# Kernel tuning notes

Measured on AMD Instinct MI355X. Metric: run time of the kernel, lower is better.

The kernel has to match this reference:

```python
import jax, jax.numpy as jnp
import numpy as np

NLAT, NLON = 361, 720
LMAX = NLAT - 1          # lobatto grid: lmax = nlat - 1
MMAX = NLON // 2 + 1     # rfft width


def setup_inputs() -> dict:
    key = jax.random.key(0)
    kx, kw = jax.random.split(key)
    x = jax.random.normal(kx, (1, 8, NLAT, NLON), dtype=jnp.float32)
    # Precomputed quadrature-weighted associated Legendre table [mmax, lmax, nlat].
    # Faithful structure: P_l^m == 0 for l < m (triangular in (m, l)).
    w = jax.random.normal(kw, (MMAX, LMAX, NLAT), dtype=jnp.float32)
    tri = (jnp.arange(LMAX)[None, :, None] >= jnp.arange(MMAX)[:, None, None])
    weights = w * tri.astype(jnp.float32)
    return {"x": x, "weights": weights}


def reference(x, weights):
    nlon = x.shape[-1]
    mmax = weights.shape[0]
    # torch.fft.rfft(..., norm='forward') scales by 1/nlon; module multiplies by 2*pi
    X = (2.0 * jnp.pi / nlon) * jnp.fft.rfft(x, axis=-1)   # [..., nlat, nlon//2+1] complex
    X = X[..., :mmax]                                       # [..., k=nlat, m=mmax]
    # out[..., l, m] = sum_k X[..., k, m] * W[m, l, k]  (applied to real & imag parts)
    out = jnp.einsum('...km,mlk->...lm', X, weights.astype(X.real.dtype))
    return out  # complex64, shape [..., lmax, mmax]
```

## Files before the change

kernel.cpp:

```cpp
#include <hip/hip_runtime.h>

#define NLAT 361
#define NLON 720
#define LMAX 360
#define MMAX 361

#define NS   6
#define QN   61
#define NN   64
#define XTQ_FLOATS (MMAX * NLAT * 8)

static constexpr float kAngF = 8.72664625997164788e-3f;

__global__ __launch_bounds__(256) void k_dft4(const float* __restrict__ x,
                                              float* __restrict__ xtq) {
    const int bx  = blockIdx.x;
    const int nq  = blockIdx.y;
    const int tid = threadIdx.x;
    const int ks  = tid >> 7;
    const int ml  = tid & 127;
    const int n0  = nq * QN;

    __shared__ __align__(16) float xe[2][NN][8];

    for (int j = tid; j < 2 * 8 * NN; j += 256) {
        int s  = j / (8 * NN);
        int r  = j - s * (8 * NN);
        int ch = r / NN;
        int nn = r - ch * NN;
        int n  = n0 + nn;
        int k  = bx * 2 + s;
        float v = 0.f;
        if (nn < QN && n <= 360 && k <= 360) {
            const float* __restrict__ row = x + ((size_t)ch * NLAT + k) * NLON;
            float a = row[n];
            float b = (n == 0) ? 0.f : row[NLON - n];
            v = a + b;
        }
        xe[s][nn][ch] = v;
    }
    __syncthreads();

    int mm[3];
    mm[0] = ml; mm[1] = ml + 128;
    const bool m2v = (ml + 256 <= 360);
    mm[2] = m2v ? (ml + 256) : 360;

    float P0[3], P1[3], c2[3];
#pragma unroll
    for (int q = 0; q < 3; ++q) {
        int m  = mm[q];
        int t0 = (n0 * m) % NLON;
        int t1 = t0 + m; if (t1 >= NLON) t1 -= NLON;
        P0[q] = cosf((float)t0 * kAngF);
        P1[q] = cosf((float)t1 * kAngF);
        c2[q] = 2.f * cosf((float)m * kAngF);
    }

    float acc[3][8];
#pragma unroll
    for (int q = 0; q < 3; ++q)
#pragma unroll
        for (int b = 0; b < 8; ++b) acc[q][b] = 0.f;

#pragma unroll 4
    for (int nn = 0; nn < NN; ++nn) {
        float4 e0 = *(const float4*)&xe[ks][nn][0];
        float4 e1 = *(const float4*)&xe[ks][nn][4];
#pragma unroll
        for (int q = 0; q < 3; ++q) {
            float f = P0[q];
            acc[q][0] += f * e0.x;  acc[q][1] += f * e0.y;
            acc[q][2] += f * e0.z;  acc[q][3] += f * e0.w;
            acc[q][4] += f * e1.x;  acc[q][5] += f * e1.y;
            acc[q][6] += f * e1.z;  acc[q][7] += f * e1.w;
            float Pn = c2[q] * P1[q] - P0[q];
            P0[q] = P1[q];
            P1[q] = Pn;
        }
    }

    if (nq == NS - 1) {
        float4 e0 = *(const float4*)&xe[ks][55][0];
        float4 e1 = *(const float4*)&xe[ks][55][4];
#pragma unroll
        for (int q = 0; q < 3; ++q) {
            float sgn = (mm[q] & 1) ? -1.f : 1.f;
            float h = 0.5f * sgn;
            acc[q][0] -= h * e0.x;  acc[q][1] -= h * e0.y;
            acc[q][2] -= h * e0.z;  acc[q][3] -= h * e0.w;
            acc[q][4] -= h * e1.x;  acc[q][5] -= h * e1.y;
            acc[q][6] -= h * e1.z;  acc[q][7] -= h * e1.w;
        }
    }

#pragma unroll
    for (int q = 0; q < 3; ++q)
#pragma unroll
        for (int b = 0; b < 8; ++b) acc[q][b] *= kAngF;

    const int k = bx * 2 + ks;
    if (k <= 360) {
        float4* __restrict__ o4 = (float4*)(xtq + (size_t)nq * XTQ_FLOATS);
        int b0 = (mm[0] * NLAT + k) * 2;
        o4[b0]     = make_float4(acc[0][0], acc[0][1], acc[0][2], acc[0][3]);
        o4[b0 + 1] = make_float4(acc[0][4], acc[0][5], acc[0][6], acc[0][7]);
        int b1 = (mm[1] * NLAT + k) * 2;
        o4[b1]     = make_float4(acc[1][0], acc[1][1], acc[1][2], acc[1][3]);
        o4[b1 + 1] = make_float4(acc[1][4], acc[1][5], acc[1][6], acc[1][7]);
        if (m2v) {
            int b2 = (mm[2] * NLAT + k) * 2;
            o4[b2]     = make_float4(acc[2][0], acc[2][1], acc[2][2], acc[2][3]);
            o4[b2 + 1] = make_float4(acc[2][4], acc[2][5], acc[2][6], acc[2][7]);
        }
    }
}

__global__ __launch_bounds__(256) void k_reduce6(const float* __restrict__ q,
                                                 float4* __restrict__ o) {
    int i = blockIdx.x * 256 + threadIdx.x;
    if (i >= XTQ_FLOATS / 4) return;
    const float4* q4 = (const float4*)q;
    float4 s = q4[i];
#pragma unroll
    for (int u = 1; u < NS; ++u) {
        float4 a = q4[i + (size_t)u * (XTQ_FLOATS / 4)];
        s.x += a.x; s.y += a.y; s.z += a.z; s.w += a.w;
    }
    o[i] = s;
}

__global__ __launch_bounds__(256) void k_contract4(const float* __restrict__ W,
                                                   const float* __restrict__ xt,
                                                   float* __restrict__ out) {
    const int lt   = blockIdx.x;
    const int mloc = blockIdx.y;
    const int m    = mloc;
    const int l0   = lt * 32;
    const int tid  = threadIdx.x;

    if (l0 + 31 < m) {
        int l = l0 + (tid >> 3), bc = tid & 7;
        out[(bc * LMAX + l) * MMAX + m] = 0.f;
        return;
    }

    const int kk = tid & 31, lq = tid >> 5;
    const int lb = l0 + lq * 4;

    int lr[4];
#pragma unroll
    for (int j = 0; j < 4; ++j) {
        int l = lb + j;
        if (l < m)        l = m;
        if (l > LMAX - 1) l = LMAX - 1;
        lr[j] = l;
    }

    const float* __restrict__ Wm = W + (size_t)m * (LMAX * NLAT);
    const float* __restrict__ r0 = Wm + lr[0] * NLAT + kk;
    const float* __restrict__ r1 = Wm + lr[1] * NLAT + kk;
    const float* __restrict__ r2 = Wm + lr[2] * NLAT + kk;
    const float* __restrict__ r3 = Wm + lr[3] * NLAT + kk;

    float wv[12][4];
#pragma unroll
    for (int t = 0; t < 11; ++t) {
        wv[t][0] = r0[t * 32];
        wv[t][1] = r1[t * 32];
        wv[t][2] = r2[t * 32];
        wv[t][3] = r3[t * 32];
    }
    {
        int kq = 11 * 32 + kk;
        int kc = (kq <= 360) ? kq : 360;
        wv[11][0] = Wm[lr[0] * NLAT + kc];
        wv[11][1] = Wm[lr[1] * NLAT + kc];
        wv[11][2] = Wm[lr[2] * NLAT + kc];
        wv[11][3] = Wm[lr[3] * NLAT + kc];
        if (kq > 360) { wv[11][0] = wv[11][1] = wv[11][2] = wv[11][3] = 0.f; }
    }

    float v[32];
#pragma unroll
    for (int i = 0; i < 32; ++i) v[i] = 0.f;

    const float4* __restrict__ xt4 = (const float4*)xt;
#pragma unroll
    for (int t = 0; t < 12; ++t) {
        int kq = t * 32 + kk;
        int kc = (kq <= 360) ? kq : 360;
        int xb = (mloc * NLAT + kc) * 2;
        float4 x0 = xt4[xb], x1 = xt4[xb + 1];
#pragma unroll
        for (int j = 0; j < 4; ++j) {
            float wj = wv[t][j];
            v[j*8 + 0] += wj * x0.x;  v[j*8 + 1] += wj * x0.y;
            v[j*8 + 2] += wj * x0.z;  v[j*8 + 3] += wj * x0.w;
            v[j*8 + 4] += wj * x1.x;  v[j*8 + 5] += wj * x1.y;
            v[j*8 + 6] += wj * x1.z;  v[j*8 + 7] += wj * x1.w;
        }
    }

#define RSTEP(MASK, CNT) { const bool hi = (kk & MASK) != 0; \
    _Pragma("unroll") \
    for (int i = 0; i < CNT; ++i) { \
        float keep = hi ? v[i + CNT] : v[i]; \
        float send = hi ? v[i] : v[i + CNT]; \
        v[i] = keep + __shfl_xor(send, MASK); } }
    RSTEP(16, 16) RSTEP(8, 8) RSTEP(4, 4) RSTEP(2, 2) RSTEP(1, 1)
#undef RSTEP

    int j  = kk >> 3;
    int bc = kk & 7;
    int l  = l0 + lq * 4 + j;
    if (l >= LMAX) return;
    float r = (l < m) ? 0.f : v[0];
    out[(bc * LMAX + l) * MMAX + m] = r;
}

template<int CPLX>
__global__ __launch_bounds__(192) void k_dft_leg(const float* __restrict__ x,
                                                 float* __restrict__ xt,
                                                 int mb, int mc) {
    const int k    = blockIdx.x;
    const int half = blockIdx.y;
    const int tid  = threadIdx.x;

    __shared__ __align__(16) float  xr[8 * 724];
    __shared__ __align__(16) float2 exo[8 * 362];

    {
        const float4* __restrict__ x4 = (const float4*)x;
        for (int j = tid; j < 8 * 180; j += 192) {
            int b = j / 180, q = j - b * 180;
            ((float4*)&xr[b * 724])[q] = x4[(b * NLAT + k) * 180 + q];
        }
        if (tid < 8) ((float4*)&xr[tid * 724])[180] = make_float4(0.f, 0.f, 0.f, 0.f);
    }
    __syncthreads();

    for (int j = tid; j < 8 * NLAT; j += 192) {
        int b = j / NLAT, n = j - b * NLAT;
        float xa  = xr[b * 724 + n];
        float xbv = xr[b * 724 + (NLON - n)];
        exo[b * 362 + n] = make_float2(xa + xbv, xa - xbv);
    }
    __syncthreads();

    const int  m_local = half * 192 + tid;
    const bool valid   = (m_local < mc);
    const int  m       = mb + (valid ? m_local : 0);

    float aRe[8], aIm[8];
#pragma unroll
    for (int b = 0; b < 8; ++b) { aRe[b] = 0.f; aIm[b] = 0.f; }

    int tacc = 0;
    for (int n = 0; n < NLAT; ++n) {
        float sn, cs;
        __sincosf((float)tacc * kAngF, &sn, &cs);
        float wgt = (n == 360) ? 0.5f : 1.0f;
        float fc = wgt * kAngF * cs;
        float fs = -wgt * kAngF * sn;
        tacc += m;
        if (tacc >= NLON) tacc -= NLON;
#pragma unroll
        for (int b = 0; b < 8; ++b) {
            float2 e = exo[b * 362 + n];
            aRe[b] += fc * e.x;
            if (CPLX) aIm[b] += fs * e.y;
        }
    }

    if (valid) {
        float4* __restrict__ xt4 = (float4*)xt;
        if (CPLX) {
            int base = (m_local * NLAT + k) * 4;
#pragma unroll
            for (int q = 0; q < 4; ++q)
                xt4[base + q] = make_float4(aRe[2*q], aIm[2*q], aRe[2*q+1], aIm[2*q+1]);
        } else {
            int base = (m_local * NLAT + k) * 2;
            xt4[base + 0] = make_float4(aRe[0], aRe[1], aRe[2], aRe[3]);
            xt4[base + 1] = make_float4(aRe[4], aRe[5], aRe[6], aRe[7]);
        }
    }
}

template<int CPLX>
__global__ __launch_bounds__(256) void k_contract_leg(const float* __restrict__ W,
                                                      const float* __restrict__ xt,
                                                      float* __restrict__ out,
                                                      int mb) {
    const int lt   = blockIdx.x;
    const int mloc = blockIdx.y;
    const int m    = mb + mloc;
    const int l0   = lt * 32;
    const int tid  = threadIdx.x;

    if (l0 + 31 < m) {
        int l = l0 + (tid >> 3), bc = tid & 7;
        int idx = (bc * LMAX + l) * MMAX + m;
        if (CPLX) ((float2*)out)[idx] = make_float2(0.f, 0.f);
        else      out[idx] = 0.f;
        return;
    }

    const int kk = tid & 31, lq = tid >> 5;
    const int lb = l0 + lq * 4;

    int lr[4];
#pragma unroll
    for (int j = 0; j < 4; ++j) {
        int l = lb + j;
        if (l < m)        l = m;
        if (l > LMAX - 1) l = LMAX - 1;
        lr[j] = l;
    }

    const float* __restrict__ Wm = W + (size_t)m * (LMAX * NLAT);
    const float4* __restrict__ xt4 = (const float4*)xt;
    constexpr int NX = CPLX ? 4 : 2;
    constexpr int NV = CPLX ? 64 : 32;

    float v[NV];
#pragma unroll
    for (int i = 0; i < NV; ++i) v[i] = 0.f;

#define CLOAD(T, WV, XV) { \
    int kq = (T) * 32 + kk; \
    int kc = (kq < NLAT) ? kq : (NLAT - 1); \
    _Pragma("unroll") \
    for (int j = 0; j < 4; ++j) WV[j] = Wm[lr[j] * NLAT + kc]; \
    int xb = (mloc * NLAT + kc) * NX; \
    _Pragma("unroll") \
    for (int q = 0; q < NX; ++q) XV[q] = xt4[xb + q]; \
    if (kq >= NLAT) { WV[0] = WV[1] = WV[2] = WV[3] = 0.f; } }

#define CFMA(WV, XV) { \
    _Pragma("unroll") \
    for (int j = 0; j < 4; ++j) { \
        float wj = WV[j]; \
        if (CPLX) { \
            _Pragma("unroll") \
            for (int q = 0; q < 4; ++q) { \
                v[j*16 + (2*q  )*2 + 0] += wj * XV[q].x; \
                v[j*16 + (2*q  )*2 + 1] += wj * XV[q].y; \
                v[j*16 + (2*q+1)*2 + 0] += wj * XV[q].z; \
                v[j*16 + (2*q+1)*2 + 1] += wj * XV[q].w; \
            } \
        } else { \
            v[j*8 + 0] += wj * XV[0].x;  v[j*8 + 1] += wj * XV[0].y; \
            v[j*8 + 2] += wj * XV[0].z;  v[j*8 + 3] += wj * XV[0].w; \
            v[j*8 + 4] += wj * XV[1].x;  v[j*8 + 5] += wj * XV[1].y; \
            v[j*8 + 6] += wj * XV[1].z;  v[j*8 + 7] += wj * XV[1].w; \
        } \
    } }

    float  w0[4], w1[4], wn[4];
    float4 x0[NX], x1[NX], xn[NX];
    CLOAD(0, w0, x0)
    CLOAD(1, w1, x1)
#pragma unroll
    for (int t = 0; t < 12; ++t) {
        if (t < 10) CLOAD(t + 2, wn, xn)
        CFMA(w0, x0)
#pragma unroll
        for (int j = 0; j < 4; ++j) w0[j] = w1[j];
#pragma unroll
        for (int q = 0; q < NX; ++q) x0[q] = x1[q];
        if (t < 10) {
#pragma unroll
            for (int j = 0; j < 4; ++j) w1[j] = wn[j];
#pragma unroll
            for (int q = 0; q < NX; ++q) x1[q] = xn[q];
        }
    }
#undef CLOAD
#undef CFMA

#define RSTEP(MASK, CNT) { const bool hi = (kk & MASK) != 0; \
    _Pragma("unroll") \
    for (int i = 0; i < CNT; ++i) { \
        float keep = hi ? v[i + CNT] : v[i]; \
        float send = hi ? v[i] : v[i + CNT]; \
        v[i] = keep + __shfl_xor(send, MASK); } }
    if (CPLX) {
        RSTEP(16, 32) RSTEP(8, 16) RSTEP(4, 8) RSTEP(2, 4) RSTEP(1, 2)
    } else {
        RSTEP(16, 16) RSTEP(8, 8) RSTEP(4, 4) RSTEP(2, 2) RSTEP(1, 1)
    }
#undef RSTEP

    int j  = kk >> 3;
    int bc = kk & 7;
    int l  = l0 + lq * 4 + j;
    if (l >= LMAX) return;
    int idx = (bc * LMAX + l) * MMAX + m;
    if (CPLX) {
        float2 r = make_float2(v[0], v[1]);
        if (l < m) r = make_float2(0.f, 0.f);
        ((float2*)out)[idx] = r;
    } else {
        float r = (l < m) ? 0.f : v[0];
        out[idx] = r;
    }
}

extern "C" void kernel_launch(void* const* d_in, const int* in_sizes, int n_in,
                              void* d_out, int out_size, void* d_ws, size_t ws_size,
                              hipStream_t stream) {
    const float* x = (const float*)d_in[0];
    const float* W = (const float*)d_in[1];
    float* ws = (float*)d_ws;

    const int n_complex = 8 * LMAX * MMAX;
    const int cplx = (out_size >= 2 * n_complex) ? 1 : 0;

    if (!cplx) {
        const size_t need = (size_t)(NS + 1) * XTQ_FLOATS * sizeof(float);
        if (ws_size >= need) {
            float* q  = ws;
            float* xt = ws + (size_t)NS * XTQ_FLOATS;
            k_dft4<<<dim3(181, NS), dim3(256), 0, stream>>>(x, q);
            k_reduce6<<<dim3((XTQ_FLOATS / 4 + 255) / 256), dim3(256), 0, stream>>>(
                q, (float4*)xt);
            k_contract4<<<dim3(12, MMAX), dim3(256), 0, stream>>>(W, xt, (float*)d_out);
            return;
        }
    }

    const int xs_per_mk = cplx ? 16 : 8;
    const size_t per_m_bytes = (size_t)NLAT * xs_per_mk * sizeof(float);
    int CM = (int)(ws_size / per_m_bytes);
    if (CM > MMAX) CM = MMAX;
    if (CM < 1)    CM = 1;
    for (int mbase = 0; mbase < MMAX; mbase += CM) {
        int mc = MMAX - mbase;
        if (mc > CM) mc = CM;
        if (cplx) {
            k_dft_leg<1><<<dim3(NLAT, (mc + 191) / 192), dim3(192), 0, stream>>>(
                x, ws, mbase, mc);
            k_contract_leg<1><<<dim3(12, mc), dim3(256), 0, stream>>>(W, ws, (float*)d_out, mbase);
        } else {
            k_dft_leg<0><<<dim3(NLAT, (mc + 191) / 192), dim3(192), 0, stream>>>(
                x, ws, mbase, mc);
            k_contract_leg<0><<<dim3(12, mc), dim3(256), 0, stream>>>(W, ws, (float*)d_out, mbase);
        }
    }
}
```

Baseline: 54.15 us.

## Split DFT work over m instead of n and drop partial-sum reduction kernel

The real DFT kernel now assigns one m per thread across 3 m-chunks and loops over all 361 n values, instead of giving each thread three m values over one of six n-slices. This removes the six-way partial buffer and the separate reduction kernel, cutting workspace traffic and one launch. The Chebyshev recurrence restarts every ~91 steps to limit error, and it uses fast __cosf. The cost is a larger shared tile per block (361 rows instead of 64) and a longer serial loop per thread with less reuse of each shared-memory load across m values.

```diff
diff --git a/kernel.cpp b/kernel.cpp
--- a/kernel.cpp
+++ b/kernel.cpp
@@ -5,129 +5,88 @@
 #define LMAX 360
 #define MMAX 361
 
-#define NS   6
-#define QN   61
-#define NN   64
-#define XTQ_FLOATS (MMAX * NLAT * 8)
+#define XT_FLOATS (MMAX * NLAT * 8)
 
 static constexpr float kAngF = 8.72664625997164788e-3f;
 
-__global__ __launch_bounds__(256) void k_dft4(const float* __restrict__ x,
-                                              float* __restrict__ xtq) {
+__global__ __launch_bounds__(256) void k_dft5(const float* __restrict__ x,
+                                              float* __restrict__ xt) {
     const int bx  = blockIdx.x;
-    const int nq  = blockIdx.y;
+    const int mc  = blockIdx.y;
     const int tid = threadIdx.x;
     const int ks  = tid >> 7;
     const int ml  = tid & 127;
-    const int n0  = nq * QN;
-
-    __shared__ __align__(16) float xe[2][NN][8];
-
-    for (int j = tid; j < 2 * 8 * NN; j += 256) {
-        int s  = j / (8 * NN);
-        int r  = j - s * (8 * NN);
-        int ch = r / NN;
-        int nn = r - ch * NN;
-        int n  = n0 + nn;
+    const int m   = mc * 128 + ml;
+    const bool mv = (m <= 360);
+    const int mm  = mv ? m : 360;
+
+    __shared__ __align__(16) float xe[2][361][12];
+
+    for (int j = tid; j < 2 * 8 * 361; j += 256) {
+        int s  = j / 2888;
+        int r  = j - s * 2888;
+        int ch = r / 361;
+        int n  = r - ch * 361;
         int k  = bx * 2 + s;
         float v = 0.f;
-        if (nn < QN && n <= 360 && k <= 360) {
+        if (k <= 360) {
             const float* __restrict__ row = x + ((size_t)ch * NLAT + k) * NLON;
             float a = row[n];
             float b = (n == 0) ? 0.f : row[NLON - n];
             v = a + b;
         }
-        xe[s][nn][ch] = v;
+        xe[s][n][ch] = v;
     }
     __syncthreads();
 
-    int mm[3];
-    mm[0] = ml; mm[1] = ml + 128;
-    const bool m2v = (ml + 256 <= 360);
-    mm[2] = m2v ? (ml + 256) : 360;
-
-    float P0[3], P1[3], c2[3];
-#pragma unroll
-    for (int q = 0; q < 3; ++q) {
-        int m  = mm[q];
-        int t0 = (n0 * m) % NLON;
-        int t1 = t0 + m; if (t1 >= NLON) t1 -= NLON;
-        P0[q] = cosf((float)t0 * kAngF);
-        P1[q] = cosf((float)t1 * kAngF);
-        c2[q] = 2.f * cosf((float)m * kAngF);
-    }
-
-    float acc[3][8];
-#pragma unroll
-    for (int q = 0; q < 3; ++q)
-#pragma unroll
-        for (int b = 0; b < 8; ++b) acc[q][b] = 0.f;
-
-#pragma unroll 4
-    for (int nn = 0; nn < NN; ++nn) {
-        float4 e0 = *(const float4*)&xe[ks][nn][0];
-        float4 e1 = *(const float4*)&xe[ks][nn][4];
-#pragma unroll
-        for (int q = 0; q < 3; ++q) {
-            float f = P0[q];
-            acc[q][0] += f * e0.x;  acc[q][1] += f * e0.y;
-            acc[q][2] += f * e0.z;  acc[q][3] += f * e0.w;
-            acc[q][4] += f * e1.x;  acc[q][5] += f * e1.y;
-            acc[q][6] += f * e1.z;  acc[q][7] += f * e1.w;
-            float Pn = c2[q] * P1[q] - P0[q];
-            P0[q] = P1[q];
-            P1[q] = Pn;
-        }
-    }
-
-    if (nq == NS - 1) {
-        float4 e0 = *(const float4*)&xe[ks][55][0];
-        float4 e1 = *(const float4*)&xe[ks][55][4];
-#pragma unroll
-        for (int q = 0; q < 3; ++q) {
-            float sgn = (mm[q] & 1) ? -1.f : 1.f;
-            float h = 0.5f * sgn;
-            acc[q][0] -= h * e0.x;  acc[q][1] -= h * e0.y;
-            acc[q][2] -= h * e0.z;  acc[q][3] -= h * e0.w;
-            acc[q][4] -= h * e1.x;  acc[q][5] -= h * e1.y;
-            acc[q][6] -= h * e1.z;  acc[q][7] -= h * e1.w;
-        }
-    }
-
-#pragma unroll
-    for (int q = 0; q < 3; ++q)
-#pragma unroll
-        for (int b = 0; b < 8; ++b) acc[q][b] *= kAngF;
+    float acc[8];
+#pragma unroll
+    for (int b = 0; b < 8; ++b) acc[b] = 0.f;
+
+    const float c2 = 2.f * __cosf((float)mm * kAngF);
+
+    const int cb[5] = {0, 91, 182, 273, 361};
+#pragma unroll
+    for (int c = 0; c < 4; ++c) {
+        const int n0 = cb[c], n1 = cb[c + 1];
+        int t0 = (n0 * mm) % NLON;
+        int t1 = t0 + mm; if (t1 >= NLON) t1 -= NLON;
+        float P0 = __cosf((float)t0 * kAngF);
+        float P1 = __cosf((float)t1 * kAngF);
+        for (int n = n0; n < n1; ++n) {
+            float4 e0 = *(const float4*)&xe[ks][n][0];
+            float4 e1 = *(const float4*)&xe[ks][n][4];
+            float f = P0;
+            acc[0] += f * e0.x;  acc[1] += f * e0.y;
+            acc[2] += f * e0.z;  acc[3] += f * e0.w;
+            acc[4] += f * e1.x;  acc[5] += f * e1.y;
+            acc[6] += f * e1.z;  acc[7] += f * e1.w;
+            float Pn = c2 * P1 - P0;
+            P0 = P1;
+            P1 = Pn;
+        }
+    }
+
+    {
+        float4 e0 = *(const float4*)&xe[ks][360][0];
+        float4 e1 = *(const float4*)&xe[ks][360][4];
+        float h = 0.5f * ((mm & 1) ? -1.f : 1.f);
+        acc[0] -= h * e0.x;  acc[1] -= h * e0.y;
+        acc[2] -= h * e0.z;  acc[3] -= h * e0.w;
+        acc[4] -= h * e1.x;  acc[5] -= h * e1.y;
+        acc[6] -= h * e1.z;  acc[7] -= h * e1.w;
+    }
+
+#pragma unroll
+    for (int b = 0; b < 8; ++b) acc[b] *= kAngF;
 
     const int k = bx * 2 + ks;
-    if (k <= 360) {
-        float4* __restrict__ o4 = (float4*)(xtq + (size_t)nq * XTQ_FLOATS);
-        int b0 = (mm[0] * NLAT + k) * 2;
-        o4[b0]     = make_float4(acc[0][0], acc[0][1], acc[0][2], acc[0][3]);
-        o4[b0 + 1] = make_float4(acc[0][4], acc[0][5], acc[0][6], acc[0][7]);
-        int b1 = (mm[1] * NLAT + k) * 2;
-        o4[b1]     = make_float4(acc[1][0], acc[1][1], acc[1][2], acc[1][3]);
-        o4[b1 + 1] = make_float4(acc[1][4], acc[1][5], acc[1][6], acc[1][7]);
-        if (m2v) {
-            int b2 = (mm[2] * NLAT + k) * 2;
-            o4[b2]     = make_float4(acc[2][0], acc[2][1], acc[2][2], acc[2][3]);
-            o4[b2 + 1] = make_float4(acc[2][4], acc[2][5], acc[2][6], acc[2][7]);
-        }
-    }
-}
-
-__global__ __launch_bounds__(256) void k_reduce6(const float* __restrict__ q,
-                                                 float4* __restrict__ o) {
-    int i = blockIdx.x * 256 + threadIdx.x;
-    if (i >= XTQ_FLOATS / 4) return;
-    const float4* q4 = (const float4*)q;
-    float4 s = q4[i];
-#pragma unroll
-    for (int u = 1; u < NS; ++u) {
-        float4 a = q4[i + (size_t)u * (XTQ_FLOATS / 4)];
-        s.x += a.x; s.y += a.y; s.z += a.z; s.w += a.w;
-    }
-    o[i] = s;
+    if (mv && k <= 360) {
+        float4* __restrict__ o4 = (float4*)xt;
+        int b0 = (m * NLAT + k) * 2;
+        o4[b0]     = make_float4(acc[0], acc[1], acc[2], acc[3]);
+        o4[b0 + 1] = make_float4(acc[4], acc[5], acc[6], acc[7]);
+    }
 }
 
 __global__ __launch_bounds__(256) void k_contract4(const float* __restrict__ W,
@@ -418,17 +377,10 @@
     const int n_complex = 8 * LMAX * MMAX;
     const int cplx = (out_size >= 2 * n_complex) ? 1 : 0;
 
-    if (!cplx) {
-        const size_t need = (size_t)(NS + 1) * XTQ_FLOATS * sizeof(float);
-        if (ws_size >= need) {
-            float* q  = ws;
-            float* xt = ws + (size_t)NS * XTQ_FLOATS;
-            k_dft4<<<dim3(181, NS), dim3(256), 0, stream>>>(x, q);
-            k_reduce6<<<dim3((XTQ_FLOATS / 4 + 255) / 256), dim3(256), 0, stream>>>(
-                q, (float4*)xt);
-            k_contract4<<<dim3(12, MMAX), dim3(256), 0, stream>>>(W, xt, (float*)d_out);
-            return;
-        }
+    if (!cplx && ws_size >= (size_t)XT_FLOATS * sizeof(float)) {
+        k_dft5<<<dim3(181, 3), dim3(256), 0, stream>>>(x, ws);
+        k_contract4<<<dim3(12, MMAX), dim3(256), 0, stream>>>(W, ws, (float*)d_out);
+        return;
     }
 
     const int xs_per_mk = cplx ? 16 : 8;
```

After: 59.68 us. 10.2% more time.

## Restructure DFT into 4 n-slices with k-major output and transpose-reduce kernel

Applied to the files above, without the earlier changes.

The DFT kernel now processes 4 latitudes per block and 6 m values per thread over 4 n-slices of 91 instead of 6 of 61. It writes k-major partials so stores are coalesced along m, and uses fast __cosf for the recurrence seeds. The separate reduce kernel is replaced by a tiled shared-memory kernel that sums the slices and transposes to the m-major layout the contraction needs. This cuts partial-sum traffic and makes the DFT stores contiguous, but uses more registers per thread and the approximate cosine may cost accuracy.

```diff
diff --git a/kernel.cpp b/kernel.cpp
--- a/kernel.cpp
+++ b/kernel.cpp
@@ -5,33 +5,33 @@
 #define LMAX 360
 #define MMAX 361
 
-#define NS   6
-#define QN   61
-#define NN   64
-#define XTQ_FLOATS (MMAX * NLAT * 8)
+#define NSL  4
+#define QSL  91
+#define SL_F (NLAT * MMAX * 8)
 
 static constexpr float kAngF = 8.72664625997164788e-3f;
 
-__global__ __launch_bounds__(256) void k_dft4(const float* __restrict__ x,
-                                              float* __restrict__ xtq) {
+__global__ __launch_bounds__(256) void k_dft7(const float* __restrict__ x,
+                                              float* __restrict__ slices) {
     const int bx  = blockIdx.x;
     const int nq  = blockIdx.y;
     const int tid = threadIdx.x;
-    const int ks  = tid >> 7;
-    const int ml  = tid & 127;
-    const int n0  = nq * QN;
-
-    __shared__ __align__(16) float xe[2][NN][8];
-
-    for (int j = tid; j < 2 * 8 * NN; j += 256) {
-        int s  = j / (8 * NN);
-        int r  = j - s * (8 * NN);
-        int ch = r / NN;
-        int nn = r - ch * NN;
+    const int w   = tid >> 6;
+    const int ml  = tid & 63;
+    const int n0  = nq * QSL;
+    const int cnt = min(QSL, NLAT - n0);
+
+    __shared__ __align__(16) float xe[4][QSL][8];
+
+    for (int j = tid; j < 4 * 8 * QSL; j += 256) {
+        int s  = j / (8 * QSL);
+        int r  = j - s * (8 * QSL);
+        int ch = r / QSL;
+        int nn = r - ch * QSL;
+        int k  = bx * 4 + s;
         int n  = n0 + nn;
-        int k  = bx * 2 + s;
         float v = 0.f;
-        if (nn < QN && n <= 360 && k <= 360) {
+        if (nn < cnt && k <= 360) {
             const float* __restrict__ row = x + ((size_t)ch * NLAT + k) * NLON;
             float a = row[n];
             float b = (n == 0) ? 0.f : row[NLON - n];
@@ -41,34 +41,29 @@
     }
     __syncthreads();
 
-    int mm[3];
-    mm[0] = ml; mm[1] = ml + 128;
-    const bool m2v = (ml + 256 <= 360);
-    mm[2] = m2v ? (ml + 256) : 360;
-
-    float P0[3], P1[3], c2[3];
-#pragma unroll
-    for (int q = 0; q < 3; ++q) {
-        int m  = mm[q];
+    float P0[6], P1[6], c2[6];
+#pragma unroll
+    for (int q = 0; q < 6; ++q) {
+        int m = ml + 64 * q; if (m > 360) m = 360;
         int t0 = (n0 * m) % NLON;
         int t1 = t0 + m; if (t1 >= NLON) t1 -= NLON;
-        P0[q] = cosf((float)t0 * kAngF);
-        P1[q] = cosf((float)t1 * kAngF);
-        c2[q] = 2.f * cosf((float)m * kAngF);
-    }
-
-    float acc[3][8];
-#pragma unroll
-    for (int q = 0; q < 3; ++q)
+        P0[q] = __cosf((float)t0 * kAngF);
+        P1[q] = __cosf((float)t1 * kAngF);
+        c2[q] = 2.f * __cosf((float)m * kAngF);
+    }
+
+    float acc[6][8];
+#pragma unroll
+    for (int q = 0; q < 6; ++q)
 #pragma unroll
         for (int b = 0; b < 8; ++b) acc[q][b] = 0.f;
 
-#pragma unroll 4
-    for (int nn = 0; nn < NN; ++nn) {
-        float4 e0 = *(const float4*)&xe[ks][nn][0];
-        float4 e1 = *(const float4*)&xe[ks][nn][4];
-#pragma unroll
-        for (int q = 0; q < 3; ++q) {
+#pragma unroll 2
+    for (int nn = 0; nn < cnt; ++nn) {
+        float4 e0 = *(const float4*)&xe[w][nn][0];
+        float4 e1 = *(const float4*)&xe[w][nn][4];
+#pragma unroll
+        for (int q = 0; q < 6; ++q) {
             float f = P0[q];
             acc[q][0] += f * e0.x;  acc[q][1] += f * e0.y;
             acc[q][2] += f * e0.z;  acc[q][3] += f * e0.w;
@@ -80,13 +75,13 @@
         }
     }
 
-    if (nq == NS - 1) {
-        float4 e0 = *(const float4*)&xe[ks][55][0];
-        float4 e1 = *(const float4*)&xe[ks][55][4];
-#pragma unroll
-        for (int q = 0; q < 3; ++q) {
-            float sgn = (mm[q] & 1) ? -1.f : 1.f;
-            float h = 0.5f * sgn;
+    if (nq == NSL - 1) {
+        float4 e0 = *(const float4*)&xe[w][87][0];
+        float4 e1 = *(const float4*)&xe[w][87][4];
+#pragma unroll
+        for (int q = 0; q < 6; ++q) {
+            int m = ml + 64 * q;
+            float h = 0.5f * ((m & 1) ? -1.f : 1.f);
             acc[q][0] -= h * e0.x;  acc[q][1] -= h * e0.y;
             acc[q][2] -= h * e0.z;  acc[q][3] -= h * e0.w;
             acc[q][4] -= h * e1.x;  acc[q][5] -= h * e1.y;
@@ -94,48 +89,69 @@
         }
     }
 
-#pragma unroll
-    for (int q = 0; q < 3; ++q)
-#pragma unroll
-        for (int b = 0; b < 8; ++b) acc[q][b] *= kAngF;
-
-    const int k = bx * 2 + ks;
+    const int k = bx * 4 + w;
     if (k <= 360) {
-        float4* __restrict__ o4 = (float4*)(xtq + (size_t)nq * XTQ_FLOATS);
-        int b0 = (mm[0] * NLAT + k) * 2;
-        o4[b0]     = make_float4(acc[0][0], acc[0][1], acc[0][2], acc[0][3]);
-        o4[b0 + 1] = make_float4(acc[0][4], acc[0][5], acc[0][6], acc[0][7]);
-        int b1 = (mm[1] * NLAT + k) * 2;
-        o4[b1]     = make_float4(acc[1][0], acc[1][1], acc[1][2], acc[1][3]);
-        o4[b1 + 1] = make_float4(acc[1][4], acc[1][5], acc[1][6], acc[1][7]);
-        if (m2v) {
-            int b2 = (mm[2] * NLAT + k) * 2;
-            o4[b2]     = make_float4(acc[2][0], acc[2][1], acc[2][2], acc[2][3]);
-            o4[b2 + 1] = make_float4(acc[2][4], acc[2][5], acc[2][6], acc[2][7]);
-        }
-    }
-}
-
-__global__ __launch_bounds__(256) void k_reduce6(const float* __restrict__ q,
-                                                 float4* __restrict__ o) {
-    int i = blockIdx.x * 256 + threadIdx.x;
-    if (i >= XTQ_FLOATS / 4) return;
-    const float4* q4 = (const float4*)q;
-    float4 s = q4[i];
-#pragma unroll
-    for (int u = 1; u < NS; ++u) {
-        float4 a = q4[i + (size_t)u * (XTQ_FLOATS / 4)];
-        s.x += a.x; s.y += a.y; s.z += a.z; s.w += a.w;
-    }
-    o[i] = s;
+        float* __restrict__ sl = slices + (size_t)nq * SL_F;
+#pragma unroll
+        for (int q = 0; q < 6; ++q) {
+            int m = ml + 64 * q;
+            if (m > 360) continue;
+            float4* o = (float4*)(sl + ((size_t)k * MMAX + m) * 8);
+            o[0] = make_float4(acc[q][0] * kAngF, acc[q][1] * kAngF,
+                               acc[q][2] * kAngF, acc[q][3] * kAngF);
+            o[1] = make_float4(acc[q][4] * kAngF, acc[q][5] * kAngF,
+                               acc[q][6] * kAngF, acc[q][7] * kAngF);
+        }
+    }
+}
+
+#define TK 16
+#define TM 32
+#define TSTRIDE 265
+__global__ __launch_bounds__(256) void k_redT(const float* __restrict__ slices,
+                                              float* __restrict__ xt) {
+    const int k0  = blockIdx.x * TK;
+    const int m0  = blockIdx.y * TM;
+    const int tid = threadIdx.x;
+
+    __shared__ __align__(16) float t[TK * TSTRIDE];
+
+    for (int j = tid; j < TK * TM * 2; j += 256) {
+        int kk = j / (TM * 2);
+        int r  = j - kk * (TM * 2);
+        int mm = r >> 1, h = r & 1;
+        int k = k0 + kk, m = m0 + mm;
+        float4 s = make_float4(0.f, 0.f, 0.f, 0.f);
+        if (k <= 360 && m <= 360) {
+            size_t off = ((size_t)k * MMAX + m) * 2 + h;
+            const float4* p = (const float4*)slices;
+#pragma unroll
+            for (int q = 0; q < NSL; ++q) {
+                float4 a = p[off + (size_t)q * (SL_F / 4)];
+                s.x += a.x; s.y += a.y; s.z += a.z; s.w += a.w;
+            }
+        }
+        *(float4*)&t[kk * TSTRIDE + mm * 8 + h * 4] = s;
+    }
+    __syncthreads();
+
+    for (int j = tid; j < TM * TK * 2; j += 256) {
+        int mm = j / (TK * 2);
+        int r  = j - mm * (TK * 2);
+        int kk = r >> 1, h = r & 1;
+        int k = k0 + kk, m = m0 + mm;
+        if (k <= 360 && m <= 360) {
+            float4 v = *(const float4*)&t[kk * TSTRIDE + mm * 8 + h * 4];
+            ((float4*)xt)[((size_t)m * MMAX + k) * 2 + h] = v;
+        }
+    }
 }
 
 __global__ __launch_bounds__(256) void k_contract4(const float* __restrict__ W,
                                                    const float* __restrict__ xt,
                                                    float* __restrict__ out) {
     const int lt   = blockIdx.x;
-    const int mloc = blockIdx.y;
-    const int m    = mloc;
+    const int m    = blockIdx.y;
     const int l0   = lt * 32;
     const int tid  = threadIdx.x;
 
@@ -190,7 +206,7 @@
     for (int t = 0; t < 12; ++t) {
         int kq = t * 32 + kk;
         int kc = (kq <= 360) ? kq : 360;
-        int xb = (mloc * NLAT + kc) * 2;
+        int xb = (m * NLAT + kc) * 2;
         float4 x0 = xt4[xb], x1 = xt4[xb + 1];
 #pragma unroll
         for (int j = 0; j < 4; ++j) {
@@ -418,17 +434,13 @@
     const int n_complex = 8 * LMAX * MMAX;
     const int cplx = (out_size >= 2 * n_complex) ? 1 : 0;
 
-    if (!cplx) {
-        const size_t need = (size_t)(NS + 1) * XTQ_FLOATS * sizeof(float);
-        if (ws_size >= need) {
-            float* q  = ws;
-            float* xt = ws + (size_t)NS * XTQ_FLOATS;
-            k_dft4<<<dim3(181, NS), dim3(256), 0, stream>>>(x, q);
-            k_reduce6<<<dim3((XTQ_FLOATS / 4 + 255) / 256), dim3(256), 0, stream>>>(
-                q, (float4*)xt);
-            k_contract4<<<dim3(12, MMAX), dim3(256), 0, stream>>>(W, xt, (float*)d_out);
-            return;
-        }
+    if (!cplx && ws_size >= (size_t)(NSL + 1) * SL_F * sizeof(float)) {
+        float* slices = ws;
+        float* xt     = ws + (size_t)NSL * SL_F;
+        k_dft7<<<dim3(91, NSL), dim3(256), 0, stream>>>(x, slices);
+        k_redT<<<dim3(23, 12), dim3(256), 0, stream>>>(slices, xt);
+        k_contract4<<<dim3(12, MMAX), dim3(256), 0, stream>>>(W, xt, (float*)d_out);
+        return;
     }
 
     const int xs_per_mk = cplx ? 16 : 8;
```

Result: slower. 58.39 us (+7.8%).
